# Kernel tuning notes

Measured on AMD Instinct MI355X. Metric: run time of the kernel, lower is better.

Reference implementation:

```python
import jax, jax.numpy as jnp
import numpy as np

H = 16  # n_heads


def setup_inputs() -> dict:
    key = jax.random.key(0)
    ks = jax.random.split(key, 12)
    B, S, D = 16, 512, 1024
    inp = {
        "query": jax.random.normal(ks[0], (B, S, D), jnp.float32),
        "key": jax.random.normal(ks[1], (B, S, D), jnp.float32),
        "value": jax.random.normal(ks[2], (B, S, D), jnp.float32),
        "mask": jnp.ones((B, S), dtype=bool),
        "adj": jax.random.uniform(ks[3], (B, S, S), jnp.float32),
        # nn.Linear weights are [out, in]; y = x @ W.T + b
        "Wq": jax.random.normal(ks[4], (D, D), jnp.float32) / np.sqrt(D),
        "bq": jnp.zeros((D,), jnp.float32),
        "Wk": jax.random.normal(ks[5], (D, D), jnp.float32) / np.sqrt(D),
        "bk": jnp.zeros((D,), jnp.float32),
        "Wv": jax.random.normal(ks[6], (D, D), jnp.float32) / np.sqrt(D),
        "bv": jnp.zeros((D,), jnp.float32),
        "Wo": jax.random.normal(ks[7], (D, D), jnp.float32) / np.sqrt(D),
        "bo": jnp.zeros((D,), jnp.float32),
        "beta": jnp.array([0.5], jnp.float32),  # learned residual scale (init 0 in torch)
    }
    return inp


def reference(query, key, value, mask, adj, Wq, bq, Wk, bk, Wv, bv, Wo, bo, beta):
    B, S, D = query.shape
    h = H
    dk = D // h
    N = S * dk  # channel-attention "sequence" length

    def proj(x, W, b):
        # [B,S,D] -> [B,h,S,dk]
        return (x @ W.T + b).reshape(B, S, h, dk).transpose(0, 2, 1, 3)

    Q = proj(query, Wq, bq)
    K = proj(key, Wk, bk)
    V = proj(value, Wv, bv)

    # Flatten each head: [B, h, S*dk]; torch's q,k,v are the [B,N,h] transposes.
    Qf = Q.reshape(B, h, N)
    Kf = K.reshape(B, h, N)
    Vf = V.reshape(B, h, N)

    # channel attention: scores = q^T k / sqrt(h) -> [B,h,h]
    scores = jnp.einsum("bin,bjn->bij", Qf, Kf) / jnp.sqrt(jnp.asarray(h, Qf.dtype))
    attn = jax.nn.softmax(scores, axis=-1)  # dropout is identity at eval

    # x2 = attn @ v^T -> [B,h,N] -> view [B,h,S,dk]
    x2 = jnp.einsum("bij,bjn->bin", attn, Vf).reshape(B, h, S, dk)

    x = V + beta * x2                      # scaled residual on value
    x = x.transpose(0, 2, 1, 3).reshape(B, S, D)
    out = x @ Wo.T + bo
    return out, attn
```

## Files before the change

### kernel.cpp

```cpp
#include <hip/hip_runtime.h>
#include <cstdint>
#include <cstddef>


#define DIM 1024

typedef _Float16 f16_t;
typedef _Float16 f16x4_t __attribute__((ext_vector_type(4)));
typedef _Float16 f16x8_t __attribute__((ext_vector_type(8)));
typedef float    f32x4_t __attribute__((ext_vector_type(4)));

__device__ __forceinline__ void async_ld16(const void* g, void* l) {
    __builtin_amdgcn_global_load_lds((const __attribute__((address_space(1))) void*)g,
                                     (__attribute__((address_space(3))) void*)l,
                                     16, 0, 0);
}

__global__ __launch_bounds__(256) void pack_w(
    const float* __restrict__ Wq, const float* __restrict__ Wk,
    const float* __restrict__ Wv, const float* __restrict__ Wo,
    f16_t* __restrict__ Bq, f16_t* __restrict__ Bk,
    f16_t* __restrict__ Bv, f16_t* __restrict__ Bo)
{
    const int u = blockIdx.x * 256 + threadIdx.x;
    const float* src; f16_t* dst; int i;
    if (u < 262144)       { src = Wq; dst = Bq; i = u; }
    else if (u < 524288)  { src = Wk; dst = Bk; i = u - 262144; }
    else if (u < 786432)  { src = Wv; dst = Bv; i = u - 524288; }
    else                  { src = Wo; dst = Bo; i = u - 786432; }
    float4 s = ((const float4*)src)[i];
    f16x4_t h;
    h[0] = (f16_t)s.x; h[1] = (f16_t)s.y; h[2] = (f16_t)s.z; h[3] = (f16_t)s.w;
    ((f16x4_t*)dst)[i] = h;
}

__device__ __forceinline__ void gemm_body_f32A(
    const float* __restrict__ A, const f16_t* __restrict__ B,
    const float* __restrict__ bias, f16_t* __restrict__ C16,
    f16_t* As, f16_t* Bs, int tileM, int tileN)
{
    const int tid  = threadIdx.x;
    const int lane = tid & 63;
    const int w    = tid >> 6;
    const int wm = (w & 1) << 6;
    const int wn = (w >> 1) << 6;

    f32x4_t acc[4][4];
#pragma unroll
    for (int i = 0; i < 4; ++i)
#pragma unroll
        for (int j = 0; j < 4; ++j)
            acc[i][j] = (f32x4_t){0.f, 0.f, 0.f, 0.f};

    const int srow = lane >> 3;
    const int scol = ((lane & 7) ^ (lane >> 3)) << 3;
    const int arow = lane & 15;
    const int sx   = lane & 7;
    const int kqu  = lane >> 4;

    int arows[4], acols[4];
#pragma unroll
    for (int s = 0; s < 4; ++s) {
        const int n = tid + (s << 8);
        arows[s] = n >> 3;
        acols[s] = ((n & 7) ^ ((n >> 3) & 7)) << 3;
    }

    for (int kt = 0; kt < 16; ++kt) {
        const int k0 = kt << 6;
#pragma unroll
        for (int t4 = 0; t4 < 4; ++t4) {
            const int row = (w << 5) + (t4 << 3);
            async_ld16(B + (size_t)(tileN + row + srow) * DIM + k0 + scol,
                       (void*)(Bs + row * 64));
        }
        float4 ld[4][2];
#pragma unroll
        for (int s = 0; s < 4; ++s) {
            const float* src = A + (size_t)(tileM + arows[s]) * DIM + k0 + acols[s];
            ld[s][0] = ((const float4*)src)[0];
            ld[s][1] = ((const float4*)src)[1];
        }
#pragma unroll
        for (int s = 0; s < 4; ++s) {
            f16x8_t h;
            h[0] = (f16_t)ld[s][0].x; h[1] = (f16_t)ld[s][0].y;
            h[2] = (f16_t)ld[s][0].z; h[3] = (f16_t)ld[s][0].w;
            h[4] = (f16_t)ld[s][1].x; h[5] = (f16_t)ld[s][1].y;
            h[6] = (f16_t)ld[s][1].z; h[7] = (f16_t)ld[s][1].w;
            *(f16x8_t*)(As + (tid + (s << 8)) * 8) = h;
        }
        __syncthreads();
#pragma unroll
        for (int kk = 0; kk < 2; ++kk) {
            const int cu = ((kk << 2) + kqu) ^ sx;
            f16x8_t af[4], bfv[4];
#pragma unroll
            for (int mt = 0; mt < 4; ++mt)
                af[mt] = *(const f16x8_t*)(As + (wm + (mt << 4) + arow) * 64 + (cu << 3));
#pragma unroll
            for (int nt = 0; nt < 4; ++nt)
                bfv[nt] = *(const f16x8_t*)(Bs + (wn + (nt << 4) + arow) * 64 + (cu << 3));
#pragma unroll
            for (int mt = 0; mt < 4; ++mt)
#pragma unroll
                for (int nt = 0; nt < 4; ++nt)
                    acc[mt][nt] = __builtin_amdgcn_mfma_f32_16x16x32_f16(
                        af[mt], bfv[nt], acc[mt][nt], 0, 0, 0);
        }
        __syncthreads();
    }

    const int rq = (lane >> 4) << 2;
#pragma unroll
    for (int nt = 0; nt < 4; ++nt) {
        const int col = tileN + wn + (nt << 4) + arow;
        const float bv = bias[col];
#pragma unroll
        for (int mt = 0; mt < 4; ++mt) {
            const int row = tileM + wm + (mt << 4) + rq;
#pragma unroll
            for (int r = 0; r < 4; ++r)
                C16[(size_t)(row + r) * DIM + col] = (f16_t)(acc[mt][nt][r] + bv);
        }
    }
}

struct Gemm3Args {
    const float* A[3];
    const f16_t* B[3];
    const float* bias[3];
    f16_t*       C16[3];
};

__global__ __launch_bounds__(256) void gemm3(Gemm3Args args)
{
    __shared__ __align__(16) f16_t As[128 * 64];
    __shared__ __align__(16) f16_t Bs[128 * 64];
    const int z = blockIdx.z;
    gemm_body_f32A(args.A[z], args.B[z], args.bias[z], args.C16[z],
                   As, Bs, blockIdx.x * 128, blockIdx.y * 128);
}

__global__ __launch_bounds__(256) void gemm_o(
    const f16_t* __restrict__ A, const f16_t* __restrict__ B,
    const float* __restrict__ bias, float* __restrict__ C)
{
    __shared__ __align__(16) f16_t As[128 * 64];
    __shared__ __align__(16) f16_t Bs[128 * 64];
    const int tileM = blockIdx.x * 128, tileN = blockIdx.y * 128;
    const int tid  = threadIdx.x;
    const int lane = tid & 63;
    const int w    = tid >> 6;
    const int wm = (w & 1) << 6;
    const int wn = (w >> 1) << 6;

    f32x4_t acc[4][4];
#pragma unroll
    for (int i = 0; i < 4; ++i)
#pragma unroll
        for (int j = 0; j < 4; ++j)
            acc[i][j] = (f32x4_t){0.f, 0.f, 0.f, 0.f};

    const int srow = lane >> 3;
    const int scol = ((lane & 7) ^ (lane >> 3)) << 3;
    const int arow = lane & 15;
    const int sx   = lane & 7;
    const int kqu  = lane >> 4;

    for (int kt = 0; kt < 16; ++kt) {
        const int k0 = kt << 6;
#pragma unroll
        for (int t4 = 0; t4 < 4; ++t4) {
            const int row = (w << 5) + (t4 << 3);
            async_ld16(A + (size_t)(tileM + row + srow) * DIM + k0 + scol,
                       (void*)(As + row * 64));
            async_ld16(B + (size_t)(tileN + row + srow) * DIM + k0 + scol,
                       (void*)(Bs + row * 64));
        }
        __syncthreads();
#pragma unroll
        for (int kk = 0; kk < 2; ++kk) {
            const int cu = ((kk << 2) + kqu) ^ sx;
            f16x8_t af[4], bfv[4];
#pragma unroll
            for (int mt = 0; mt < 4; ++mt)
                af[mt] = *(const f16x8_t*)(As + (wm + (mt << 4) + arow) * 64 + (cu << 3));
#pragma unroll
            for (int nt = 0; nt < 4; ++nt)
                bfv[nt] = *(const f16x8_t*)(Bs + (wn + (nt << 4) + arow) * 64 + (cu << 3));
#pragma unroll
            for (int mt = 0; mt < 4; ++mt)
#pragma unroll
                for (int nt = 0; nt < 4; ++nt)
                    acc[mt][nt] = __builtin_amdgcn_mfma_f32_16x16x32_f16(
                        af[mt], bfv[nt], acc[mt][nt], 0, 0, 0);
        }
        __syncthreads();
    }

    const int rq = (lane >> 4) << 2;
#pragma unroll
    for (int nt = 0; nt < 4; ++nt) {
        const int col = tileN + wn + (nt << 4) + arow;
        const float bv = bias[col];
#pragma unroll
        for (int mt = 0; mt < 4; ++mt) {
            const int row = tileM + wm + (mt << 4) + rq;
#pragma unroll
            for (int r = 0; r < 4; ++r)
                C[(size_t)(row + r) * DIM + col] = acc[mt][nt][r] + bv;
        }
    }
}

__global__ __launch_bounds__(256) void scores_kernel(
    const f16_t* __restrict__ Pq16, const f16_t* __restrict__ Pk16,
    float* __restrict__ part)
{
    __shared__ float red[4][256];
    const int b = blockIdx.x;
    const int slice = blockIdx.y;
    const int lane = threadIdx.x & 63;
    const int w = threadIdx.x >> 6;
    const int m  = lane & 15;
    const int q8 = (lane >> 4) << 3;

    f32x4_t acc = (f32x4_t){0.f, 0.f, 0.f, 0.f};
    const int s0 = slice * 32 + w * 8;
#pragma unroll
    for (int ss = 0; ss < 8; ++ss) {
        const size_t rb = (size_t)(b * 512 + s0 + ss) * DIM;
        const f16_t* qrow = Pq16 + rb;
        const f16_t* krow = Pk16 + rb;
#pragma unroll
        for (int c0 = 0; c0 < 64; c0 += 32) {
            f16x8_t af = *(const f16x8_t*)(qrow + m * 64 + c0 + q8);
            f16x8_t bf = *(const f16x8_t*)(krow + m * 64 + c0 + q8);
            acc = __builtin_amdgcn_mfma_f32_16x16x32_f16(af, bf, acc, 0, 0, 0);
        }
    }
    const int rq = (lane >> 4) << 2;
#pragma unroll
    for (int r = 0; r < 4; ++r)
        red[w][(rq + r) * 16 + m] = acc[r];
    __syncthreads();
    const int t = threadIdx.x;
    part[(size_t)(b * 16 + slice) * 256 + t] =
        red[0][t] + red[1][t] + red[2][t] + red[3][t];
}

__global__ __launch_bounds__(256) void mix_kernel(
    const f16_t* __restrict__ Pv16, const float* __restrict__ part,
    const float* __restrict__ beta_p,
    float* __restrict__ attn_out, f16_t* __restrict__ xmix)
{
    __shared__ float Msh[256];
    const int rbase = blockIdx.x * 8;
    const int b = rbase >> 9;
    const int t = threadIdx.x;
    if (t < 16) {
        const int i = t;
        float s[16];
#pragma unroll
        for (int j = 0; j < 16; ++j) s[j] = 0.f;
#pragma unroll 4
        for (int sl = 0; sl < 16; ++sl) {
            const float* pp = part + (size_t)(b * 16 + sl) * 256 + i * 16;
#pragma unroll
            for (int j4 = 0; j4 < 4; ++j4) {
                float4 v4 = ((const float4*)pp)[j4];
                s[j4 * 4 + 0] += v4.x; s[j4 * 4 + 1] += v4.y;
                s[j4 * 4 + 2] += v4.z; s[j4 * 4 + 3] += v4.w;
            }
        }
        float mx = -1e30f;
#pragma unroll
        for (int j = 0; j < 16; ++j) {
            s[j] *= 0.25f;
            mx = fmaxf(mx, s[j]);
        }
        float sum = 0.f;
#pragma unroll
        for (int j = 0; j < 16; ++j) { s[j] = expf(s[j] - mx); sum += s[j]; }
        const float inv = 1.f / sum;
        const float beta = beta_p[0];
        const bool wr_attn = (blockIdx.x & 63) == 0;
#pragma unroll
        for (int j = 0; j < 16; ++j) {
            float a = s[j] * inv;
            if (wr_attn) attn_out[(b * 16 + i) * 16 + j] = a;
            Msh[i * 16 + j] = beta * a + ((j == i) ? 1.f : 0.f);
        }
    }
    __syncthreads();
    const int w = threadIdx.x >> 6;
    const int lane = threadIdx.x & 63;
#pragma unroll
    for (int rr = 0; rr < 2; ++rr) {
        const int r = rbase + w * 2 + rr;
        const f16_t* vrow = Pv16 + (size_t)r * DIM;
        float v[16];
#pragma unroll
        for (int j = 0; j < 16; ++j) v[j] = (float)vrow[j * 64 + lane];
#pragma unroll
        for (int i = 0; i < 16; ++i) {
            float x = 0.f;
#pragma unroll
            for (int j = 0; j < 16; ++j) x += Msh[i * 16 + j] * v[j];
            xmix[(size_t)r * DIM + i * 64 + lane] = (f16_t)x;
        }
    }
}

extern "C" void kernel_launch(void* const* d_in, const int* in_sizes, int n_in,
                              void* d_out, int out_size, void* d_ws, size_t ws_size,
                              hipStream_t stream)
{
    (void)in_sizes; (void)n_in; (void)out_size; (void)ws_size;
    const float* q    = (const float*)d_in[0];
    const float* k    = (const float*)d_in[1];
    const float* v    = (const float*)d_in[2];
    const float* Wq   = (const float*)d_in[5];
    const float* bq   = (const float*)d_in[6];
    const float* Wk   = (const float*)d_in[7];
    const float* bk   = (const float*)d_in[8];
    const float* Wv   = (const float*)d_in[9];
    const float* bv   = (const float*)d_in[10];
    const float* Wo   = (const float*)d_in[11];
    const float* bo   = (const float*)d_in[12];
    const float* beta = (const float*)d_in[13];

    float* out  = (float*)d_out;
    float* attn = (float*)d_out + 8388608;

    char* p = (char*)d_ws;
    auto take = [&](size_t n) -> char* {
        char* cur = p; p += (n + 255) & ~(size_t)255; return cur;
    };
    f16_t* Bq = (f16_t*)take(2097152);
    f16_t* Bk = (f16_t*)take(2097152);
    f16_t* Bv = (f16_t*)take(2097152);
    f16_t* Bo = (f16_t*)take(2097152);
    f16_t* Pq16 = (f16_t*)take(16777216);
    f16_t* Pk16 = (f16_t*)take(16777216);
    f16_t* Pv16 = (f16_t*)take(16777216);
    f16_t* xmix = (f16_t*)take(16777216);
    float* part = (float*)take(262144);

    pack_w<<<4096, 256, 0, stream>>>(Wq, Wk, Wv, Wo, Bq, Bk, Bv, Bo);

    Gemm3Args ga;
    ga.A[0] = q; ga.A[1] = k; ga.A[2] = v;
    ga.B[0] = Bq; ga.B[1] = Bk; ga.B[2] = Bv;
    ga.bias[0] = bq; ga.bias[1] = bk; ga.bias[2] = bv;
    ga.C16[0] = Pq16; ga.C16[1] = Pk16; ga.C16[2] = Pv16;
    gemm3<<<dim3(64, 8, 3), 256, 0, stream>>>(ga);

    scores_kernel<<<dim3(16, 16), 256, 0, stream>>>(Pq16, Pk16, part);
    mix_kernel<<<1024, 256, 0, stream>>>(Pv16, part, beta, attn, xmix);
    gemm_o<<<dim3(64, 8), 256, 0, stream>>>(xmix, Bo, bo, out);
}
```

Before: 297.6 us.

## Async-load fp32 activations to LDS in QKV GEMM and vectorize mix kernel

The QKV GEMM now streams fp32 A tiles straight into LDS with global_load_lds, using an XOR swizzle, and converts them to fp16 when building fragments. This replaces the register round-trip load, convert and store, which should overlap A loads better. LDS use doubles (32KB for A), which may lower occupancy. The mix kernel processes 16 rows per block with 8-wide f16 vector loads and stores, and pack_w converts 8 elements per thread.

```diff
diff --git a/kernel.cpp b/kernel.cpp
--- a/kernel.cpp
+++ b/kernel.cpp
@@ -24,20 +24,22 @@
 {
     const int u = blockIdx.x * 256 + threadIdx.x;
     const float* src; f16_t* dst; int i;
-    if (u < 262144)       { src = Wq; dst = Bq; i = u; }
-    else if (u < 524288)  { src = Wk; dst = Bk; i = u - 262144; }
-    else if (u < 786432)  { src = Wv; dst = Bv; i = u - 524288; }
-    else                  { src = Wo; dst = Bo; i = u - 786432; }
-    float4 s = ((const float4*)src)[i];
-    f16x4_t h;
-    h[0] = (f16_t)s.x; h[1] = (f16_t)s.y; h[2] = (f16_t)s.z; h[3] = (f16_t)s.w;
-    ((f16x4_t*)dst)[i] = h;
-}
-
-__device__ __forceinline__ void gemm_body_f32A(
+    if (u < 131072)       { src = Wq; dst = Bq; i = u; }
+    else if (u < 262144)  { src = Wk; dst = Bk; i = u - 131072; }
+    else if (u < 393216)  { src = Wv; dst = Bv; i = u - 262144; }
+    else                  { src = Wo; dst = Bo; i = u - 393216; }
+    float4 s0 = ((const float4*)src)[2 * i];
+    float4 s1 = ((const float4*)src)[2 * i + 1];
+    f16x8_t h;
+    h[0] = (f16_t)s0.x; h[1] = (f16_t)s0.y; h[2] = (f16_t)s0.z; h[3] = (f16_t)s0.w;
+    h[4] = (f16_t)s1.x; h[5] = (f16_t)s1.y; h[6] = (f16_t)s1.z; h[7] = (f16_t)s1.w;
+    ((f16x8_t*)dst)[i] = h;
+}
+
+__device__ __forceinline__ void gemm_body_qkv(
     const float* __restrict__ A, const f16_t* __restrict__ B,
     const float* __restrict__ bias, f16_t* __restrict__ C16,
-    f16_t* As, f16_t* Bs, int tileM, int tileN)
+    float* As32, f16_t* Bs, int tileM, int tileN)
 {
     const int tid  = threadIdx.x;
     const int lane = tid & 63;
@@ -54,17 +56,12 @@
 
     const int srow = lane >> 3;
     const int scol = ((lane & 7) ^ (lane >> 3)) << 3;
+    const int rlo = (w << 2) + (lane >> 4);
+    const int gu  = (lane & 15) ^ rlo;
+    const float* srcA0 = A + (size_t)(tileM + rlo) * DIM + (gu << 2);
     const int arow = lane & 15;
+    const int kqu  = lane >> 4;
     const int sx   = lane & 7;
-    const int kqu  = lane >> 4;
-
-    int arows[4], acols[4];
-#pragma unroll
-    for (int s = 0; s < 4; ++s) {
-        const int n = tid + (s << 8);
-        arows[s] = n >> 3;
-        acols[s] = ((n & 7) ^ ((n >> 3) & 7)) << 3;
-    }
 
     for (int kt = 0; kt < 16; ++kt) {
         const int k0 = kt << 6;
@@ -74,30 +71,30 @@
             async_ld16(B + (size_t)(tileN + row + srow) * DIM + k0 + scol,
                        (void*)(Bs + row * 64));
         }
-        float4 ld[4][2];
-#pragma unroll
-        for (int s = 0; s < 4; ++s) {
-            const float* src = A + (size_t)(tileM + arows[s]) * DIM + k0 + acols[s];
-            ld[s][0] = ((const float4*)src)[0];
-            ld[s][1] = ((const float4*)src)[1];
-        }
-#pragma unroll
-        for (int s = 0; s < 4; ++s) {
-            f16x8_t h;
-            h[0] = (f16_t)ld[s][0].x; h[1] = (f16_t)ld[s][0].y;
-            h[2] = (f16_t)ld[s][0].z; h[3] = (f16_t)ld[s][0].w;
-            h[4] = (f16_t)ld[s][1].x; h[5] = (f16_t)ld[s][1].y;
-            h[6] = (f16_t)ld[s][1].z; h[7] = (f16_t)ld[s][1].w;
-            *(f16x8_t*)(As + (tid + (s << 8)) * 8) = h;
-        }
+#pragma unroll
+        for (int s = 0; s < 8; ++s)
+            async_ld16(srcA0 + (size_t)(s << 4) * DIM + k0,
+                       (void*)(As32 + (s << 10) + (w << 8)));
         __syncthreads();
 #pragma unroll
         for (int kk = 0; kk < 2; ++kk) {
             const int cu = ((kk << 2) + kqu) ^ sx;
+            const int U0 = (kk << 3) + (kqu << 1);
+            const int S0 = U0 ^ arow;
+            const int S1 = (U0 + 1) ^ arow;
             f16x8_t af[4], bfv[4];
 #pragma unroll
-            for (int mt = 0; mt < 4; ++mt)
-                af[mt] = *(const f16x8_t*)(As + (wm + (mt << 4) + arow) * 64 + (cu << 3));
+            for (int mt = 0; mt < 4; ++mt) {
+                const float* rb = As32 + (wm + (mt << 4) + arow) * 64;
+                f32x4_t lo = *(const f32x4_t*)(rb + (S0 << 2));
+                f32x4_t hi = *(const f32x4_t*)(rb + (S1 << 2));
+                f16x8_t h;
+                h[0] = (f16_t)lo[0]; h[1] = (f16_t)lo[1];
+                h[2] = (f16_t)lo[2]; h[3] = (f16_t)lo[3];
+                h[4] = (f16_t)hi[0]; h[5] = (f16_t)hi[1];
+                h[6] = (f16_t)hi[2]; h[7] = (f16_t)hi[3];
+                af[mt] = h;
+            }
 #pragma unroll
             for (int nt = 0; nt < 4; ++nt)
                 bfv[nt] = *(const f16x8_t*)(Bs + (wn + (nt << 4) + arow) * 64 + (cu << 3));
@@ -135,11 +132,11 @@
 
 __global__ __launch_bounds__(256) void gemm3(Gemm3Args args)
 {
-    __shared__ __align__(16) f16_t As[128 * 64];
+    __shared__ __align__(16) float As32[128 * 64];
     __shared__ __align__(16) f16_t Bs[128 * 64];
     const int z = blockIdx.z;
-    gemm_body_f32A(args.A[z], args.B[z], args.bias[z], args.C16[z],
-                   As, Bs, blockIdx.x * 128, blockIdx.y * 128);
+    gemm_body_qkv(args.A[z], args.B[z], args.bias[z], args.C16[z],
+                  As32, Bs, blockIdx.x * 128, blockIdx.y * 128);
 }
 
 __global__ __launch_bounds__(256) void gemm_o(
@@ -256,8 +253,8 @@
     float* __restrict__ attn_out, f16_t* __restrict__ xmix)
 {
     __shared__ float Msh[256];
-    const int rbase = blockIdx.x * 8;
-    const int b = rbase >> 9;
+    const int rbase = blockIdx.x * 16;
+    const int b = blockIdx.x >> 5;
     const int t = threadIdx.x;
     if (t < 16) {
         const int i = t;
@@ -285,7 +282,7 @@
         for (int j = 0; j < 16; ++j) { s[j] = expf(s[j] - mx); sum += s[j]; }
         const float inv = 1.f / sum;
         const float beta = beta_p[0];
-        const bool wr_attn = (blockIdx.x & 63) == 0;
+        const bool wr_attn = (blockIdx.x & 31) == 0;
 #pragma unroll
         for (int j = 0; j < 16; ++j) {
             float a = s[j] * inv;
@@ -294,22 +291,34 @@
         }
     }
     __syncthreads();
-    const int w = threadIdx.x >> 6;
-    const int lane = threadIdx.x & 63;
-#pragma unroll
-    for (int rr = 0; rr < 2; ++rr) {
-        const int r = rbase + w * 2 + rr;
-        const f16_t* vrow = Pv16 + (size_t)r * DIM;
-        float v[16];
-#pragma unroll
-        for (int j = 0; j < 16; ++j) v[j] = (float)vrow[j * 64 + lane];
-#pragma unroll
-        for (int i = 0; i < 16; ++i) {
-            float x = 0.f;
-#pragma unroll
-            for (int j = 0; j < 16; ++j) x += Msh[i * 16 + j] * v[j];
-            xmix[(size_t)r * DIM + i * 64 + lane] = (f16_t)x;
-        }
+    const int u    = t & 7;
+    const int i8   = (t >> 3) & 1;
+    const int rloc = t >> 4;
+    const int r = rbase + rloc;
+    const f16_t* vrow = Pv16 + (size_t)r * DIM + u * 8;
+    f16x8_t v[16];
+#pragma unroll
+    for (int j = 0; j < 16; ++j)
+        v[j] = *(const f16x8_t*)(vrow + j * 64);
+    f16_t* orow = xmix + (size_t)r * DIM + u * 8;
+#pragma unroll
+    for (int ii = 0; ii < 8; ++ii) {
+        const int i = i8 * 8 + ii;
+        const float* mrow = Msh + i * 16;
+        float acc[8];
+#pragma unroll
+        for (int c = 0; c < 8; ++c) acc[c] = 0.f;
+#pragma unroll
+        for (int j = 0; j < 16; ++j) {
+            const float m = mrow[j];
+#pragma unroll
+            for (int c = 0; c < 8; ++c)
+                acc[c] += m * (float)v[j][c];
+        }
+        f16x8_t o;
+#pragma unroll
+        for (int c = 0; c < 8; ++c) o[c] = (f16_t)acc[c];
+        *(f16x8_t*)(orow + i * 64) = o;
     }
 }
 
@@ -348,7 +357,7 @@
     f16_t* xmix = (f16_t*)take(16777216);
     float* part = (float*)take(262144);
 
-    pack_w<<<4096, 256, 0, stream>>>(Wq, Wk, Wv, Wo, Bq, Bk, Bv, Bo);
+    pack_w<<<2048, 256, 0, stream>>>(Wq, Wk, Wv, Wo, Bq, Bk, Bv, Bo);
 
     Gemm3Args ga;
     ga.A[0] = q; ga.A[1] = k; ga.A[2] = v;
@@ -358,6 +367,6 @@
     gemm3<<<dim3(64, 8, 3), 256, 0, stream>>>(ga);
 
     scores_kernel<<<dim3(16, 16), 256, 0, stream>>>(Pq16, Pk16, part);
-    mix_kernel<<<1024, 256, 0, stream>>>(Pv16, part, beta, attn, xmix);
+    mix_kernel<<<512, 256, 0, stream>>>(Pv16, part, beta, attn, xmix);
     gemm_o<<<dim3(64, 8), 256, 0, stream>>>(xmix, Bo, bo, out);
 }
```

Measured after the change: 275.1 us (median of 2 runs). 1.08x faster.
